# Performance work log

Measured on AMD Instinct MI355X. Metric: run time of the kernel, lower is better.

Reference implementation:

```python
import jax, jax.numpy as jnp
import numpy as np

SIZE = 128
DELTA = 1.0
NUM_SHELLS = SIZE // 2  # 64 shells up to Nyquist; corners beyond Nyquist are discarded
DROP_DC = False
ALPHA = None
EPS = 1e-8


def _make_shell_idx(n, delta):
    # integer-frequency radial coordinate, same grid as torch.fft.fftfreq(n)*n
    f = np.fft.fftfreq(n) * n
    fx, fy, fz = np.meshgrid(f, f, f, indexing="ij")
    r = np.sqrt(fx * fx + fy * fy + fz * fz)
    idx = np.floor(r / delta).astype(np.int32)
    # voxels past the Nyquist shell go to a discard bucket (index NUM_SHELLS)
    idx = np.where(idx < NUM_SHELLS, idx, NUM_SHELLS)
    return idx


def setup_inputs() -> dict:
    key = jax.random.key(0)
    k1, k2 = jax.random.split(key)
    shape = (8, 1, SIZE, SIZE, SIZE)
    img_ref = jax.random.normal(k1, shape, dtype=jnp.float32)
    img_pred = jax.random.normal(k2, shape, dtype=jnp.float32)
    shell_idx = jnp.asarray(_make_shell_idx(SIZE, DELTA))
    return {"img_ref": img_ref, "img_pred": img_pred, "shell_idx": shell_idx}


def reference(img_ref, img_pred, shell_idx):
    B = img_ref.shape[0] * img_ref.shape[1]
    V = SIZE * SIZE * SIZE
    F1 = jnp.fft.fftn(img_ref, axes=(-3, -2, -1)).reshape(B, V)
    F2 = jnp.fft.fftn(img_pred, axes=(-3, -2, -1)).reshape(B, V)
    idx = shell_idx.reshape(V)

    # per-shell reductions (single pass, replaces num_shells dense mask-multiplies)
    cross = (F1 * jnp.conj(F2)).real          # Re sum F1 conj(F2) per shell
    p1 = (F1.real ** 2 + F1.imag ** 2)
    p2 = (F2.real ** 2 + F2.imag ** 2)

    seg = jax.vmap(lambda x: jax.ops.segment_sum(x, idx, num_segments=NUM_SHELLS + 1))
    num = seg(cross)[:, :NUM_SHELLS]          # [B, num_shells], drop discard bucket
    d1 = seg(p1)[:, :NUM_SHELLS]
    d2 = seg(p2)[:, :NUM_SHELLS]

    fsc = num / (jnp.sqrt(d1 * d2) + EPS)     # [B, num_shells]

    if ALPHA is not None:
        freq = (jnp.arange(NUM_SHELLS, dtype=jnp.float32) + 0.5) * DELTA / SIZE
        fsc = fsc * (freq ** ALPHA)
    if DROP_DC:
        fsc = fsc[:, 1:]

    loss = 1.0 - jnp.mean(fsc ** 2)
    return loss
```

## Files before the change

### kernel.cpp

```cpp
#include <hip/hip_runtime.h>
#include <math.h>

#define N      128
#define LOGN   7
#define NSQ    (N * N)
#define VOL    (N * N * N)
#define NSHELL 64
#define BTOT   8
#define FPI    3.14159265358979323846f

#define TL     16
#define TP     (TL + 1)

__device__ inline float2* fft16(float2* A, float2* B, int t) {
    const int j5 = t & 31;
    const int lg = (t >> 5) << 1;
    float2* src = A;
    float2* dst = B;
#pragma unroll
    for (int s = 0; s < 6; s += 2) {
        const int Ns = 1 << s;
        const int m  = j5 & (Ns - 1);
        const int cc = j5 >> s;
        const int e0 = (cc << (s + 2)) + m;
        float s2, c2;
        __sincosf(-FPI * (float)m / (float)(2 * Ns), &s2, &c2);
        const float cw = c2 * c2 - s2 * s2;
        const float sw = 2.f * c2 * s2;
        __syncthreads();
#pragma unroll
        for (int l = 0; l < 2; ++l) {
            const int line = lg + l;
            const float2 a  = src[ j5       * TP + line];
            const float2 cv = src[(j5 + 32) * TP + line];
            const float2 b  = src[(j5 + 64) * TP + line];
            const float2 d  = src[(j5 + 96) * TP + line];
            const float wbx = b.x * cw - b.y * sw, wby = b.x * sw + b.y * cw;
            const float wdx = d.x * cw - d.y * sw, wdy = d.x * sw + d.y * cw;
            const float Apx = a.x + wbx, Apy = a.y + wby;
            const float Amx = a.x - wbx, Amy = a.y - wby;
            const float Bpx = cv.x + wdx, Bpy = cv.y + wdy;
            const float Bmx = cv.x - wdx, Bmy = cv.y - wdy;
            const float t0x = Bpx * c2 - Bpy * s2, t0y = Bpx * s2 + Bpy * c2;
            const float t1x = Bmx * c2 - Bmy * s2, t1y = Bmx * s2 + Bmy * c2;
            dst[(e0)          * TP + line] = make_float2(Apx + t0x, Apy + t0y);
            dst[(e0 + Ns)     * TP + line] = make_float2(Amx + t1y, Amy - t1x);
            dst[(e0 + 2 * Ns) * TP + line] = make_float2(Apx - t0x, Apy - t0y);
            dst[(e0 + 3 * Ns) * TP + line] = make_float2(Amx - t1y, Amy + t1x);
        }
        float2* tmp = src; src = dst; dst = tmp;
    }
    {
        const int m   = t & 63;
        const int grp = (t >> 6) << 2;
        float sw, cw;
        __sincosf(-FPI * (float)m / 64.f, &sw, &cw);
        __syncthreads();
#pragma unroll
        for (int l = 0; l < 4; ++l) {
            const int line = grp + l;
            const float2 v0 = src[m * TP + line];
            const float2 v1 = src[(m + 64) * TP + line];
            const float wx = v1.x * cw - v1.y * sw;
            const float wy = v1.x * sw + v1.y * cw;
            dst[m * TP + line]        = make_float2(v0.x + wx, v0.y + wy);
            dst[(m + 64) * TP + line] = make_float2(v0.x - wx, v0.y - wy);
        }
    }
    __syncthreads();
    return dst;
}

__global__ __launch_bounds__(256) void k_fftz_pack(const float* __restrict__ ref,
                                                   const float* __restrict__ pred,
                                                   float2* __restrict__ Z, int b0) {
    __shared__ float2 A[N * TP], B[N * TP];
    const int t  = threadIdx.x;
    const int yt = blockIdx.x & 7;
    const int x  = (blockIdx.x >> 3) & (N - 1);
    const int bl = blockIdx.x >> 10;
    const size_t inbase = (size_t)(b0 + bl) * VOL + (size_t)x * NSQ + (size_t)yt * TL * N;
    const size_t zbase  = (size_t)bl * VOL + (size_t)x * NSQ + (size_t)yt * TL * N;
#pragma unroll
    for (int i = 0; i < 8; ++i) {
        const int elem = i * 256 + t;
        const int z = elem & (N - 1);
        const int j = elem >> LOGN;
        A[z * TP + j] = make_float2(ref[inbase + elem], pred[inbase + elem]);
    }
    float2* res = fft16(A, B, t);
#pragma unroll
    for (int i = 0; i < 8; ++i) {
        const int elem = i * 256 + t;
        const int z = elem & (N - 1);
        const int j = elem >> LOGN;
        Z[zbase + elem] = res[z * TP + j];
    }
}

__global__ __launch_bounds__(256) void k_ffty(float2* __restrict__ Z) {
    __shared__ float2 A[N * TP], B[N * TP];
    const int t   = threadIdx.x;
    const int zt  = blockIdx.x & 7;
    const int mid = (blockIdx.x >> 3) & (N - 1);
    const int bl  = blockIdx.x >> 10;
    const size_t base = (size_t)bl * VOL + (size_t)mid * NSQ + (size_t)zt * TL;
#pragma unroll
    for (int i = 0; i < 8; ++i) {
        const int elem = i * 256 + t;
        const int zz = elem & (TL - 1);
        const int j  = elem >> 4;
        A[j * TP + zz] = Z[base + (size_t)j * N + zz];
    }
    float2* res = fft16(A, B, t);
#pragma unroll
    for (int i = 0; i < 8; ++i) {
        const int elem = i * 256 + t;
        const int zz = elem & (TL - 1);
        const int j  = elem >> 4;
        Z[base + (size_t)j * N + zz] = res[j * TP + zz];
    }
}

__device__ inline int isqrt_i(int r2) {
    int s = (int)sqrtf((float)r2);
    s -= (s * s > r2);
    s += ((s + 1) * (s + 1) <= r2);
    return s;
}

__global__ __launch_bounds__(256) void k_fftx_reduce(const float2* __restrict__ Z,
                                                     float* __restrict__ accum, int b0) {
    const int t  = threadIdx.x;
    const int zr = blockIdx.x & 7;
    const int y  = (blockIdx.x >> 3) & (N - 1);
    const int bl = blockIdx.x >> 10;
    const int z0 = zr * 8;
    const int fy = y - ((y >= 64) ? N : 0);

    if (fy * fy + z0 * z0 >= 4096) return;

    __shared__ float2 A[N * TP], B[N * TP];
    __shared__ float sh[4 * 193];
    for (int i = t; i < 4 * 193; i += 256) sh[i] = 0.f;

    const int my = (N - y) & (N - 1);
    const size_t zb    = (size_t)bl * VOL;
    const size_t baseA = zb + (size_t)y  * N + z0;
    const size_t baseB = zb + (size_t)my * N;
#pragma unroll
    for (int i = 0; i < 4; ++i) {
        const int elem = i * 256 + t;
        const int zz = elem & 7;
        const int j  = elem >> 3;
        A[j * TP + zz] = Z[baseA + (size_t)j * NSQ + zz];
    }
#pragma unroll
    for (int i = 0; i < 4; ++i) {
        const int elem = i * 256 + t;
        const int zz = elem & 7;
        const int j  = elem >> 3;
        const int mz = (N - z0 - zz) & (N - 1);
        A[j * TP + 8 + zz] = Z[baseB + (size_t)j * NSQ + mz];
    }

    float2* res = fft16(A, B, t);

    const int l  = t >> 5;
    const int x0 = (t & 31) * 4;
    const int z  = z0 + l;
    const float w = (z == 0) ? 1.f : 2.f;
    const int ryz = fy * fy + z * z;
    float* bins = sh + (t & 3) * 193;

    float aC = 0.f, aP1 = 0.f, aP2 = 0.f;
    int cs = -1;
#pragma unroll
    for (int i = 0; i < 4; ++i) {
        const int x  = x0 + i;
        const int fx = x - ((x >= 64) ? N : 0);
        const int s  = isqrt_i(fx * fx + ryz);
        if (s != cs) {
            if (cs >= 0 && cs < NSHELL) {
                atomicAdd(&bins[cs * 3 + 0], w * aC);
                atomicAdd(&bins[cs * 3 + 1], w * aP1);
                atomicAdd(&bins[cs * 3 + 2], w * aP2);
            }
            cs = s; aC = 0.f; aP1 = 0.f; aP2 = 0.f;
        }
        if (s < NSHELL) {
            const int mx = (N - x) & (N - 1);
            const float2 Av = res[x  * TP + l];
            const float2 Bv = res[mx * TP + 8 + l];
            const float F1x = 0.5f * (Av.x + Bv.x);
            const float F1y = 0.5f * (Av.y - Bv.y);
            const float F2x = 0.5f * (Av.y + Bv.y);
            const float F2y = 0.5f * (Bv.x - Av.x);
            aC  += F1x * F2x + F1y * F2y;
            aP1 += F1x * F1x + F1y * F1y;
            aP2 += F2x * F2x + F2y * F2y;
        }
    }
    if (cs >= 0 && cs < NSHELL) {
        atomicAdd(&bins[cs * 3 + 0], w * aC);
        atomicAdd(&bins[cs * 3 + 1], w * aP1);
        atomicAdd(&bins[cs * 3 + 2], w * aP2);
    }
    __syncthreads();

    float* acc = accum + (size_t)(b0 + bl) * (NSHELL * 3);
    for (int i = t; i < NSHELL * 3; i += 256) {
        const float v = sh[i] + sh[193 + i] + sh[2 * 193 + i] + sh[3 * 193 + i];
        atomicAdd(&acc[i], v);
    }
}

__global__ __launch_bounds__(512) void k_final(const float* __restrict__ accum,
                                               float* __restrict__ out) {
    __shared__ float red[8];
    const int tid = threadIdx.x;
    const float* a = accum + (size_t)tid * 3;
    const float fsc = a[0] / (sqrtf(a[1] * a[2]) + 1e-8f);
    float v = fsc * fsc;
#pragma unroll
    for (int off = 32; off > 0; off >>= 1) v += __shfl_down(v, off);
    if ((tid & 63) == 0) red[tid >> 6] = v;
    __syncthreads();
    if (tid == 0) {
        float ssum = 0.f;
#pragma unroll
        for (int i = 0; i < 8; ++i) ssum += red[i];
        out[0] = 1.0f - ssum / 512.0f;
    }
}

extern "C" void kernel_launch(void* const* d_in, const int* in_sizes, int n_in,
                              void* d_out, int out_size, void* d_ws, size_t ws_size,
                              hipStream_t stream) {
    const float* ref  = (const float*)d_in[0];
    const float* pred = (const float*)d_in[1];
    float* out = (float*)d_out;

    char*   ws    = (char*)d_ws;
    float*  accum = (float*)ws;
    float2* Zbuf  = (float2*)(ws + 8192);

    const size_t zbytes = (size_t)VOL * sizeof(float2);
    int cap = 1;
    if (ws_size > 8192) {
        size_t c = (ws_size - 8192) / zbytes;
        cap = (c < 1) ? 1 : (c > BTOT ? BTOT : (int)c);
    }

    hipMemsetAsync(accum, 0, BTOT * NSHELL * 3 * sizeof(float), stream);

    for (int b0 = 0; b0 < BTOT; b0 += cap) {
        const int nb = (BTOT - b0 < cap) ? (BTOT - b0) : cap;
        const int nblk = nb * 1024;
        k_fftz_pack<<<nblk, 256, 0, stream>>>(ref, pred, Zbuf, b0);
        k_ffty<<<nblk, 256, 0, stream>>>(Zbuf);
        k_fftx_reduce<<<nblk, 256, 0, stream>>>(Zbuf, accum, b0);
    }
    k_final<<<1, 512, 0, stream>>>(accum, out);
}
```

Before: 323.9 us.

## Make shared-memory FFT in-place and vectorize global loads/stores

The ping-pong A/B shared buffers are replaced by a single in-place buffer: each radix stage loads operands into registers, syncs, then writes back. This halves LDS use per block, which allows more resident blocks per CU, at the cost of an extra barrier per stage. Global loads and stores in the z/y FFT kernels and the reduce kernel's first load now use float4 accesses, and the reduce kernel uses two shared bin copies instead of four.

```diff
diff --git a/kernel.cpp b/kernel.cpp
--- a/kernel.cpp
+++ b/kernel.cpp
@@ -12,11 +12,9 @@
 #define TL     16
 #define TP     (TL + 1)
 
-__device__ inline float2* fft16(float2* A, float2* B, int t) {
+__device__ inline void fft16_ip(float2* S, int t) {
     const int j5 = t & 31;
     const int lg = (t >> 5) << 1;
-    float2* src = A;
-    float2* dst = B;
 #pragma unroll
     for (int s = 0; s < 6; s += 2) {
         const int Ns = 1 << s;
@@ -28,27 +26,31 @@
         const float cw = c2 * c2 - s2 * s2;
         const float sw = 2.f * c2 * s2;
         __syncthreads();
+        float2 a[2], cv[2], b[2], d[2];
+#pragma unroll
+        for (int l = 0; l < 2; ++l) {
+            a[l]  = S[ j5       * TP + lg + l];
+            cv[l] = S[(j5 + 32) * TP + lg + l];
+            b[l]  = S[(j5 + 64) * TP + lg + l];
+            d[l]  = S[(j5 + 96) * TP + lg + l];
+        }
+        __syncthreads();
 #pragma unroll
         for (int l = 0; l < 2; ++l) {
             const int line = lg + l;
-            const float2 a  = src[ j5       * TP + line];
-            const float2 cv = src[(j5 + 32) * TP + line];
-            const float2 b  = src[(j5 + 64) * TP + line];
-            const float2 d  = src[(j5 + 96) * TP + line];
-            const float wbx = b.x * cw - b.y * sw, wby = b.x * sw + b.y * cw;
-            const float wdx = d.x * cw - d.y * sw, wdy = d.x * sw + d.y * cw;
-            const float Apx = a.x + wbx, Apy = a.y + wby;
-            const float Amx = a.x - wbx, Amy = a.y - wby;
-            const float Bpx = cv.x + wdx, Bpy = cv.y + wdy;
-            const float Bmx = cv.x - wdx, Bmy = cv.y - wdy;
+            const float wbx = b[l].x * cw - b[l].y * sw, wby = b[l].x * sw + b[l].y * cw;
+            const float wdx = d[l].x * cw - d[l].y * sw, wdy = d[l].x * sw + d[l].y * cw;
+            const float Apx = a[l].x + wbx, Apy = a[l].y + wby;
+            const float Amx = a[l].x - wbx, Amy = a[l].y - wby;
+            const float Bpx = cv[l].x + wdx, Bpy = cv[l].y + wdy;
+            const float Bmx = cv[l].x - wdx, Bmy = cv[l].y - wdy;
             const float t0x = Bpx * c2 - Bpy * s2, t0y = Bpx * s2 + Bpy * c2;
             const float t1x = Bmx * c2 - Bmy * s2, t1y = Bmx * s2 + Bmy * c2;
-            dst[(e0)          * TP + line] = make_float2(Apx + t0x, Apy + t0y);
-            dst[(e0 + Ns)     * TP + line] = make_float2(Amx + t1y, Amy - t1x);
-            dst[(e0 + 2 * Ns) * TP + line] = make_float2(Apx - t0x, Apy - t0y);
-            dst[(e0 + 3 * Ns) * TP + line] = make_float2(Amx - t1y, Amy + t1x);
-        }
-        float2* tmp = src; src = dst; dst = tmp;
+            S[(e0)          * TP + line] = make_float2(Apx + t0x, Apy + t0y);
+            S[(e0 + Ns)     * TP + line] = make_float2(Amx + t1y, Amy - t1x);
+            S[(e0 + 2 * Ns) * TP + line] = make_float2(Apx - t0x, Apy - t0y);
+            S[(e0 + 3 * Ns) * TP + line] = make_float2(Amx - t1y, Amy + t1x);
+        }
     }
     {
         const int m   = t & 63;
@@ -56,69 +58,88 @@
         float sw, cw;
         __sincosf(-FPI * (float)m / 64.f, &sw, &cw);
         __syncthreads();
+        float2 v0[4], v1[4];
 #pragma unroll
         for (int l = 0; l < 4; ++l) {
-            const int line = grp + l;
-            const float2 v0 = src[m * TP + line];
-            const float2 v1 = src[(m + 64) * TP + line];
-            const float wx = v1.x * cw - v1.y * sw;
-            const float wy = v1.x * sw + v1.y * cw;
-            dst[m * TP + line]        = make_float2(v0.x + wx, v0.y + wy);
-            dst[(m + 64) * TP + line] = make_float2(v0.x - wx, v0.y - wy);
+            v0[l] = S[ m       * TP + grp + l];
+            v1[l] = S[(m + 64) * TP + grp + l];
+        }
+        __syncthreads();
+#pragma unroll
+        for (int l = 0; l < 4; ++l) {
+            const float wx = v1[l].x * cw - v1[l].y * sw;
+            const float wy = v1[l].x * sw + v1[l].y * cw;
+            S[ m       * TP + grp + l] = make_float2(v0[l].x + wx, v0[l].y + wy);
+            S[(m + 64) * TP + grp + l] = make_float2(v0[l].x - wx, v0[l].y - wy);
         }
     }
     __syncthreads();
-    return dst;
 }
 
 __global__ __launch_bounds__(256) void k_fftz_pack(const float* __restrict__ ref,
                                                    const float* __restrict__ pred,
                                                    float2* __restrict__ Z, int b0) {
-    __shared__ float2 A[N * TP], B[N * TP];
+    __shared__ float2 S[N * TP];
     const int t  = threadIdx.x;
     const int yt = blockIdx.x & 7;
     const int x  = (blockIdx.x >> 3) & (N - 1);
     const int bl = blockIdx.x >> 10;
     const size_t inbase = (size_t)(b0 + bl) * VOL + (size_t)x * NSQ + (size_t)yt * TL * N;
     const size_t zbase  = (size_t)bl * VOL + (size_t)x * NSQ + (size_t)yt * TL * N;
-#pragma unroll
-    for (int i = 0; i < 8; ++i) {
-        const int elem = i * 256 + t;
+    const float4* r4 = (const float4*)(ref + inbase);
+    const float4* p4 = (const float4*)(pred + inbase);
+#pragma unroll
+    for (int i = 0; i < 2; ++i) {
+        const int idx = i * 256 + t;
+        const float4 rv = r4[idx];
+        const float4 pv = p4[idx];
+        const int elem = idx * 4;
         const int z = elem & (N - 1);
         const int j = elem >> LOGN;
-        A[z * TP + j] = make_float2(ref[inbase + elem], pred[inbase + elem]);
-    }
-    float2* res = fft16(A, B, t);
-#pragma unroll
-    for (int i = 0; i < 8; ++i) {
-        const int elem = i * 256 + t;
+        S[(z + 0) * TP + j] = make_float2(rv.x, pv.x);
+        S[(z + 1) * TP + j] = make_float2(rv.y, pv.y);
+        S[(z + 2) * TP + j] = make_float2(rv.z, pv.z);
+        S[(z + 3) * TP + j] = make_float2(rv.w, pv.w);
+    }
+    fft16_ip(S, t);
+    float4* z4 = (float4*)(Z + zbase);
+#pragma unroll
+    for (int i = 0; i < 4; ++i) {
+        const int idx = i * 256 + t;
+        const int elem = idx * 2;
         const int z = elem & (N - 1);
         const int j = elem >> LOGN;
-        Z[zbase + elem] = res[z * TP + j];
+        const float2 u0 = S[ z      * TP + j];
+        const float2 u1 = S[(z + 1) * TP + j];
+        z4[idx] = make_float4(u0.x, u0.y, u1.x, u1.y);
     }
 }
 
 __global__ __launch_bounds__(256) void k_ffty(float2* __restrict__ Z) {
-    __shared__ float2 A[N * TP], B[N * TP];
+    __shared__ float2 S[N * TP];
     const int t   = threadIdx.x;
     const int zt  = blockIdx.x & 7;
     const int mid = (blockIdx.x >> 3) & (N - 1);
     const int bl  = blockIdx.x >> 10;
     const size_t base = (size_t)bl * VOL + (size_t)mid * NSQ + (size_t)zt * TL;
 #pragma unroll
-    for (int i = 0; i < 8; ++i) {
-        const int elem = i * 256 + t;
-        const int zz = elem & (TL - 1);
-        const int j  = elem >> 4;
-        A[j * TP + zz] = Z[base + (size_t)j * N + zz];
-    }
-    float2* res = fft16(A, B, t);
-#pragma unroll
-    for (int i = 0; i < 8; ++i) {
-        const int elem = i * 256 + t;
-        const int zz = elem & (TL - 1);
-        const int j  = elem >> 4;
-        Z[base + (size_t)j * N + zz] = res[j * TP + zz];
+    for (int i = 0; i < 4; ++i) {
+        const int idx = i * 256 + t;
+        const int j = idx >> 3;
+        const int q = (idx & 7) * 2;
+        const float4 v = *(const float4*)&Z[base + (size_t)j * N + q];
+        S[j * TP + q]     = make_float2(v.x, v.y);
+        S[j * TP + q + 1] = make_float2(v.z, v.w);
+    }
+    fft16_ip(S, t);
+#pragma unroll
+    for (int i = 0; i < 4; ++i) {
+        const int idx = i * 256 + t;
+        const int j = idx >> 3;
+        const int q = (idx & 7) * 2;
+        const float2 u0 = S[j * TP + q];
+        const float2 u1 = S[j * TP + q + 1];
+        *(float4*)&Z[base + (size_t)j * N + q] = make_float4(u0.x, u0.y, u1.x, u1.y);
     }
 }
 
@@ -140,20 +161,22 @@
 
     if (fy * fy + z0 * z0 >= 4096) return;
 
-    __shared__ float2 A[N * TP], B[N * TP];
-    __shared__ float sh[4 * 193];
-    for (int i = t; i < 4 * 193; i += 256) sh[i] = 0.f;
+    __shared__ float2 S[N * TP];
+    __shared__ float sh[2 * 193];
+    for (int i = t; i < 2 * 193; i += 256) sh[i] = 0.f;
 
     const int my = (N - y) & (N - 1);
     const size_t zb    = (size_t)bl * VOL;
     const size_t baseA = zb + (size_t)y  * N + z0;
     const size_t baseB = zb + (size_t)my * N;
 #pragma unroll
-    for (int i = 0; i < 4; ++i) {
-        const int elem = i * 256 + t;
-        const int zz = elem & 7;
-        const int j  = elem >> 3;
-        A[j * TP + zz] = Z[baseA + (size_t)j * NSQ + zz];
+    for (int i = 0; i < 2; ++i) {
+        const int idx = i * 256 + t;
+        const int j = idx >> 2;
+        const int q = (idx & 3) * 2;
+        const float4 v = *(const float4*)&Z[baseA + (size_t)j * NSQ + q];
+        S[j * TP + q]     = make_float2(v.x, v.y);
+        S[j * TP + q + 1] = make_float2(v.z, v.w);
     }
 #pragma unroll
     for (int i = 0; i < 4; ++i) {
@@ -161,17 +184,17 @@
         const int zz = elem & 7;
         const int j  = elem >> 3;
         const int mz = (N - z0 - zz) & (N - 1);
-        A[j * TP + 8 + zz] = Z[baseB + (size_t)j * NSQ + mz];
-    }
-
-    float2* res = fft16(A, B, t);
+        S[j * TP + 8 + zz] = Z[baseB + (size_t)j * NSQ + mz];
+    }
+
+    fft16_ip(S, t);
 
     const int l  = t >> 5;
     const int x0 = (t & 31) * 4;
     const int z  = z0 + l;
     const float w = (z == 0) ? 1.f : 2.f;
     const int ryz = fy * fy + z * z;
-    float* bins = sh + (t & 3) * 193;
+    float* bins = sh + (t & 1) * 193;
 
     float aC = 0.f, aP1 = 0.f, aP2 = 0.f;
     int cs = -1;
@@ -190,8 +213,8 @@
         }
         if (s < NSHELL) {
             const int mx = (N - x) & (N - 1);
-            const float2 Av = res[x  * TP + l];
-            const float2 Bv = res[mx * TP + 8 + l];
+            const float2 Av = S[x  * TP + l];
+            const float2 Bv = S[mx * TP + 8 + l];
             const float F1x = 0.5f * (Av.x + Bv.x);
             const float F1y = 0.5f * (Av.y - Bv.y);
             const float F2x = 0.5f * (Av.y + Bv.y);
@@ -210,8 +233,7 @@
 
     float* acc = accum + (size_t)(b0 + bl) * (NSHELL * 3);
     for (int i = t; i < NSHELL * 3; i += 256) {
-        const float v = sh[i] + sh[193 + i] + sh[2 * 193 + i] + sh[3 * 193 + i];
-        atomicAdd(&acc[i], v);
+        atomicAdd(&acc[i], sh[i] + sh[193 + i]);
     }
 }
 
```

After: 322.9 us. About the same (-0.3%).
